# Kernel optimization log

Hardware: AMD Instinct MI355X
Metric: run time of the kernel (lower is better)

The kernel has to match this reference:

```python
import jax, jax.numpy as jnp
import numpy as np

BT, NQ, NC, C, H, HID = 192, 64, 1024, 384, 8, 1536
DH = C // H                       # 48
SCALE = DH ** -0.5
MAX_NEG = -float(np.finfo(np.float32).max)


def _ln(x, eps, g=None, b=None):
    m = x.mean(-1, keepdims=True)
    v = ((x - m) ** 2).mean(-1, keepdims=True)
    y = (x - m) / jnp.sqrt(v + eps)
    if g is not None:
        y = y * g + b
    return y


def _gelu_tanh(x):
    # GELU(approximate='tanh')
    return 0.5 * x * (1.0 + jnp.tanh(jnp.sqrt(2.0 / jnp.pi) * (x + 0.044715 * x ** 3)))


def setup_inputs() -> dict:
    key = jax.random.key(0)
    ks = jax.random.split(key, 10)
    s = lambda fan: 1.0 / np.sqrt(fan)
    return {
        "x": jax.random.normal(ks[0], (BT, NQ, C), jnp.float32),
        "context": jax.random.normal(ks[1], (BT, NC, C), jnp.float32),
        "mask": jax.random.randint(ks[2], (BT, NQ), 0, 2) > 0,
        "Wq": jax.random.normal(ks[3], (C, C), jnp.float32) * s(C),
        "bq": jnp.zeros((C,), jnp.float32),
        "Wkv": jax.random.normal(ks[4], (C, 2 * C), jnp.float32) * s(C),
        "bkv": jnp.zeros((2 * C,), jnp.float32),
        "Wo": jax.random.normal(ks[5], (C, C), jnp.float32) * s(C),
        "bo": jnp.zeros((C,), jnp.float32),
        "g_ctx": jnp.ones((C,), jnp.float32),
        "b_ctx": jnp.zeros((C,), jnp.float32),
        "W1": jax.random.normal(ks[6], (C, HID), jnp.float32) * s(C),
        "b1": jnp.zeros((HID,), jnp.float32),
        "W2": jax.random.normal(ks[7], (HID, C), jnp.float32) * s(HID),
        "b2": jnp.zeros((C,), jnp.float32),
    }


def reference(x, context, mask, Wq, bq, Wkv, bkv, Wo, bo, g_ctx, b_ctx, W1, b1, W2, b2):
    # --- cross-attention branch ---
    xn = _ln(x, 1e-6)                       # norm1 (no affine)
    cn = _ln(context, 1e-5, g_ctx, b_ctx)   # norm_context (affine, default eps)
    q = (xn @ Wq + bq).reshape(BT, NQ, H, DH).transpose(0, 2, 1, 3)    # (B,H,NQ,DH)
    kv = cn @ Wkv + bkv
    k, v = jnp.split(kv, 2, axis=-1)
    k = k.reshape(BT, NC, H, DH).transpose(0, 2, 1, 3)                 # (B,H,NC,DH)
    v = v.reshape(BT, NC, H, DH).transpose(0, 2, 1, 3)
    sim = jnp.einsum('bhqd,bhkd->bhqk', q, k) * SCALE                  # (B,H,NQ,NC)
    # mask shape (BT, NQ): True = keep query row; ~mask * (-max) bias
    bias = jnp.where(mask[:, None, :, None], 0.0, MAX_NEG)
    attn = jax.nn.softmax(sim + bias, axis=-1)
    o = jnp.einsum('bhqk,bhkd->bhqd', attn, v).transpose(0, 2, 1, 3).reshape(BT, NQ, C)
    x = x + o @ Wo + bo
    # --- MLP branch ---
    xn2 = _ln(x, 1e-6)                      # norm2 (no affine)
    x = x + _gelu_tanh(xn2 @ W1 + b1) @ W2 + b2
    return x
```

## Files before the change

kernel.cpp:

```cpp
#include <hip/hip_runtime.h>
#include <hip/hip_bf16.h>
#include <math.h>

typedef unsigned int  u32;
typedef unsigned short u16;
typedef unsigned char u8;

#define BTn   192
#define NQn   64
#define NCn   1024
#define Cd    384
#define Hn    8
#define DHn   48
#define HIDn  1536
#define ROWSX (BTn*NQn)
#define ROWSC (BTn*NCn)
#define ATT_SCALE 0.14433756729740643f

typedef __bf16 bf16x8 __attribute__((ext_vector_type(8)));
typedef float  f32x4  __attribute__((ext_vector_type(4)));

#define GLL16(gp, lp) __builtin_amdgcn_global_load_lds( \
    (const __attribute__((address_space(1))) void*)(gp), \
    (__attribute__((address_space(3))) void*)(lp), 16, 0, 0)

__device__ __forceinline__ float bf2f(u32 u) {
  union { u32 i; float f; } v; v.i = u << 16; return v.f;
}
__device__ __forceinline__ u16 f2bf(float f) {
  union { float f; u32 i; } v; v.f = f;
  u32 x = v.i;
  x += 0x7fffu + ((x >> 16) & 1u);
  return (u16)(x >> 16);
}
__device__ __forceinline__ void decode8(uint4 r, float* v) {
  v[0]=bf2f(r.x & 0xffffu); v[1]=bf2f(r.x >> 16);
  v[2]=bf2f(r.y & 0xffffu); v[3]=bf2f(r.y >> 16);
  v[4]=bf2f(r.z & 0xffffu); v[5]=bf2f(r.z >> 16);
  v[6]=bf2f(r.w & 0xffffu); v[7]=bf2f(r.w >> 16);
}
__device__ __forceinline__ float gelu_f(float x) {
  float x3 = x*x*x;
  float z = 0.7978845608028654f*x + 0.035677408136300125f*x3;
  float e = __expf(2.f*z);
  float th = 1.f - 2.f/(e+1.f);
  return 0.5f*x*(1.f+th);
}

__global__ void decode_mask_kernel(const u8* __restrict__ m, u8* __restrict__ keep) {
  __shared__ int flags[3];
  int t = threadIdx.x;
  if (t < 3) flags[t] = 0;
  __syncthreads();
  int nonbin = 0, oddset = 0, low01 = 0;
  for (int i = t; i < ROWSX; i += 256) {
    u32 b = m[i];
    if (b > 1u) nonbin = 1;
    if ((i & 3) && b) oddset = 1;
    if (((i & 3) < 2) && b) low01 = 1;
  }
  if (nonbin) flags[0] = 1;
  if (oddset) flags[1] = 1;
  if (low01)  flags[2] = 1;
  __syncthreads();
  int mode = flags[0] ? (flags[2] ? 2 : 3) : (flags[1] ? 1 : 0);
  for (int i = t; i < ROWSX; i += 256) {
    u8 k;
    if (mode == 2)      k = (m[2*i] | m[2*i+1]) ? 1 : 0;
    else if (mode == 3) k = (((const float*)m)[i] != 0.f) ? 1 : 0;
    else if (mode == 1) k = m[i] ? 1 : 0;
    else                k = (((const int*)m)[i] != 0) ? 1 : 0;
    keep[i] = k;
  }
}

template<int AFF, int SRCF32>
__global__ __launch_bounds__(256) void lnorm_kernel(
    const void* __restrict__ srcv, const float* __restrict__ gw,
    const float* __restrict__ bw, u16* __restrict__ dst, float eps)
{
  const int row  = blockIdx.x * 4 + (threadIdx.x >> 6);
  const int lane = threadIdx.x & 63;
  float v[6];
  if (SRCF32) {
    const float2* p = (const float2*)((const float*)srcv + (size_t)row*Cd);
    #pragma unroll
    for (int i = 0; i < 3; i++) { float2 u = p[lane + 64*i]; v[2*i]=u.x; v[2*i+1]=u.y; }
  } else {
    const u32* p = (const u32*)((const u16*)srcv + (size_t)row*Cd);
    #pragma unroll
    for (int i = 0; i < 3; i++) { u32 u = p[lane + 64*i]; v[2*i]=bf2f(u&0xffffu); v[2*i+1]=bf2f(u>>16); }
  }
  float s  = v[0]+v[1]+v[2]+v[3]+v[4]+v[5];
  float s2 = v[0]*v[0]+v[1]*v[1]+v[2]*v[2]+v[3]*v[3]+v[4]*v[4]+v[5]*v[5];
  #pragma unroll
  for (int o = 32; o >= 1; o >>= 1) { s += __shfl_xor(s, o); s2 += __shfl_xor(s2, o); }
  float mean = s * (1.0f/Cd);
  float var  = s2 * (1.0f/Cd) - mean*mean;
  var = var > 0.f ? var : 0.f;
  float rstd = rsqrtf(var + eps);
  u32* d32 = (u32*)(dst + (size_t)row*Cd);
  #pragma unroll
  for (int i = 0; i < 3; i++) {
    float y0 = (v[2*i]   - mean) * rstd;
    float y1 = (v[2*i+1] - mean) * rstd;
    if (AFF) {
      float2 gg = *(const float2*)(gw + 2*(lane + 64*i));
      float2 bb = *(const float2*)(bw + 2*(lane + 64*i));
      y0 = y0*gg.x + bb.x;
      y1 = y1*gg.y + bb.y;
    }
    d32[lane + 64*i] = (u32)f2bf(y0) | ((u32)f2bf(y1) << 16);
  }
}

struct WPack {
  const float* W[5];
  u16* WT[5];
  int K[5];
  int N[5];
  int off[6];
};
__global__ __launch_bounds__(256) void wconvt_all_kernel(WPack p) {
  __shared__ u16 tile[64][66];
  const int bid = blockIdx.x;
  int s = 0;
  #pragma unroll
  for (int i = 1; i < 5; i++) if (bid >= p.off[i]) s = i;
  const float* W = p.W[s];
  u16* WT = p.WT[s];
  const int K = p.K[s], N = p.N[s];
  const int lb = bid - p.off[s];
  const int t  = threadIdx.x;
  const int nt = N >> 6;
  const int bk = lb / nt, bn = lb % nt;
  const int q  = t >> 6;
  const int nl = t & 63;
  #pragma unroll
  for (int r = 0; r < 16; r++) {
    int k = q*16 + r;
    tile[nl][k] = f2bf(W[(size_t)(bk*64 + k)*N + bn*64 + nl]);
  }
  __syncthreads();
  #pragma unroll
  for (int r = 0; r < 16; r++) {
    int n = q*16 + r;
    WT[(size_t)(bn*64 + n)*K + bk*64 + nl] = tile[n][nl];
  }
}

template<int GEL, int RES, int RF32, int OF32>
__global__ __launch_bounds__(256) void mgemm_kernel(
    const u16* __restrict__ A, const u16* __restrict__ WT,
    const float* __restrict__ bias, const void* __restrict__ resv,
    void* __restrict__ Coutv, int M, int N, int K, int nx)
{
  __shared__ u16 As[3][4096];
  __shared__ u16 Bs[3][4096];
  const int t = threadIdx.x;
  const int w = t >> 6, l = t & 63, l15 = l & 15, g = l >> 4;

  const int nwg = gridDim.x;
  const int bid = blockIdx.x;
  const int wg  = (bid & 7) * (nwg >> 3) + (bid >> 3);
  const int n0 = (wg % nx) * 128, m0 = (wg / nx) * 128;
  const int wm = (w & 1) * 64, wn = (w >> 1) * 64;

  const int arow = t >> 2;
  const int swk  = (t >> 3) & 3;
  const int acol = ((t & 3) ^ swk) * 8;
  const u16* Ag = A  + (size_t)(m0 + arow) * K + acol;
  const u16* Wg = WT + (size_t)(n0 + arow) * K + acol;
  const size_t rowskip = (size_t)64 * K;

  const int xk   = (l15 >> 1) & 3;
  const int goff = ((g ^ xk) << 3);

  f32x4 acc[4][4];
  #pragma unroll
  for (int i = 0; i < 4; i++)
    #pragma unroll
    for (int j = 0; j < 4; j++) acc[i][j] = (f32x4){0.f, 0.f, 0.f, 0.f};

  const int nIter = K >> 5;

#define STAGE(nb, kk) do { \
    GLL16(Ag + (kk),           &As[nb][t*8]); \
    GLL16(Ag + (kk) + rowskip, &As[nb][2048 + t*8]); \
    GLL16(Wg + (kk),           &Bs[nb][t*8]); \
    GLL16(Wg + (kk) + rowskip, &Bs[nb][2048 + t*8]); \
  } while (0)

#define BODY(BUF, IT) do { \
    const int it_ = (IT); \
    if (it_ + 2 < nIter) { \
      STAGE((BUF + 2) % 3, (it_ + 2) << 5); \
      asm volatile("s_waitcnt vmcnt(8)" ::: "memory"); \
    } else if (it_ + 1 < nIter) { \
      asm volatile("s_waitcnt vmcnt(4)" ::: "memory"); \
    } else { \
      asm volatile("s_waitcnt vmcnt(0)" ::: "memory"); \
    } \
    __builtin_amdgcn_s_barrier(); \
    __builtin_amdgcn_sched_barrier(0); \
    { \
      bf16x8 af[4], bfv[4]; \
      _Pragma("unroll") \
      for (int i = 0; i < 4; i++) \
        af[i] = *(const bf16x8*)&As[BUF][(wm + i*16 + l15)*32 + goff]; \
      _Pragma("unroll") \
      for (int j = 0; j < 4; j++) \
        bfv[j] = *(const bf16x8*)&Bs[BUF][(wn + j*16 + l15)*32 + goff]; \
      _Pragma("unroll") \
      for (int i = 0; i < 4; i++) \
        _Pragma("unroll") \
        for (int j = 0; j < 4; j++) \
          acc[i][j] = __builtin_amdgcn_mfma_f32_16x16x32_bf16(bfv[j], af[i], acc[i][j], 0, 0, 0); \
    } \
    __builtin_amdgcn_sched_barrier(0); \
    __builtin_amdgcn_s_barrier(); \
  } while (0)

  STAGE(0, 0);
  STAGE(1, 32);
  for (int it0 = 0; it0 < nIter; it0 += 3) {
    BODY(0, it0);
    BODY(1, it0 + 1);
    BODY(2, it0 + 2);
  }
#undef BODY
#undef STAGE

  const float* resf = (const float*)resv;
  const u16*   resb = (const u16*)resv;
  float* Cf = (float*)Coutv;
  u16*   Cb = (u16*)Coutv;
  #pragma unroll
  for (int j = 0; j < 4; j++) {
    const int nb = n0 + wn + j*16 + g*4;
    const float4 bv = *(const float4*)&bias[nb];
    #pragma unroll
    for (int i = 0; i < 4; i++) {
      const int m = m0 + wm + i*16 + l15;
      float c0 = acc[i][j][0] + bv.x;
      float c1 = acc[i][j][1] + bv.y;
      float c2 = acc[i][j][2] + bv.z;
      float c3 = acc[i][j][3] + bv.w;
      if (GEL) { c0 = gelu_f(c0); c1 = gelu_f(c1); c2 = gelu_f(c2); c3 = gelu_f(c3); }
      if (RES) {
        if (RF32) {
          float4 r = *(const float4*)&resf[(size_t)m*N + nb];
          c0 += r.x; c1 += r.y; c2 += r.z; c3 += r.w;
        } else {
          uint2 r = *(const uint2*)&resb[(size_t)m*N + nb];
          c0 += bf2f(r.x & 0xffffu); c1 += bf2f(r.x >> 16);
          c2 += bf2f(r.y & 0xffffu); c3 += bf2f(r.y >> 16);
        }
      }
      if (OF32) {
        *(float4*)&Cf[(size_t)m*N + nb] = make_float4(c0, c1, c2, c3);
      } else {
        uint2 pk = make_uint2((u32)f2bf(c0) | ((u32)f2bf(c1) << 16),
                              (u32)f2bf(c2) | ((u32)f2bf(c3) << 16));
        *(uint2*)&Cb[(size_t)m*N + nb] = pk;
      }
    }
  }
}

template<int GEL, int RES, int RF32, int OF32>
__global__ __launch_bounds__(512, 4) void mgemm256_kernel(
    const u16* __restrict__ A, const u16* __restrict__ WT,
    const float* __restrict__ bias, const void* __restrict__ resv,
    void* __restrict__ Coutv, int M, int N, int K, int nx)
{
  __shared__ u16 As[3][4096];
  __shared__ u16 Bs[3][8192];
  const int t = threadIdx.x;
  const int w = t >> 6, l = t & 63, l15 = l & 15, g = l >> 4;

  const int nwg = gridDim.x;
  const int bid = blockIdx.x;
  const int wg  = (bid & 7) * (nwg >> 3) + (bid >> 3);
  const int n0 = (wg % nx) * 256, m0 = (wg / nx) * 128;
  const int wm = (w & 1) * 64, wn = (w >> 1) * 64;

  const int arow = t >> 2;
  const int swk  = (t >> 3) & 3;
  const int acol = ((t & 3) ^ swk) * 8;
  const u16* Ag = A  + (size_t)(m0 + arow) * K + acol;
  const u16* Wg = WT + (size_t)(n0 + arow) * K + acol;
  const size_t rowskipB = (size_t)128 * K;

  const int xk   = (l15 >> 1) & 3;
  const int goff = ((g ^ xk) << 3);

  f32x4 acc[4][4];
  #pragma unroll
  for (int i = 0; i < 4; i++)
    #pragma unroll
    for (int j = 0; j < 4; j++) acc[i][j] = (f32x4){0.f, 0.f, 0.f, 0.f};

  const int nIter = K >> 5;

#define STAGE(nb, kk) do { \
    GLL16(Ag + (kk),            &As[nb][t*8]); \
    GLL16(Wg + (kk),            &Bs[nb][t*8]); \
    GLL16(Wg + (kk) + rowskipB, &Bs[nb][4096 + t*8]); \
  } while (0)

#define BODY(BUF, IT) do { \
    const int it_ = (IT); \
    if (it_ + 2 < nIter) { \
      STAGE((BUF + 2) % 3, (it_ + 2) << 5); \
      asm volatile("s_waitcnt vmcnt(6)" ::: "memory"); \
    } else if (it_ + 1 < nIter) { \
      asm volatile("s_waitcnt vmcnt(3)" ::: "memory"); \
    } else { \
      asm volatile("s_waitcnt vmcnt(0)" ::: "memory"); \
    } \
    __builtin_amdgcn_s_barrier(); \
    __builtin_amdgcn_sched_barrier(0); \
    { \
      bf16x8 af[4], bfv[4]; \
      _Pragma("unroll") \
      for (int i = 0; i < 4; i++) \
        af[i] = *(const bf16x8*)&As[BUF][(wm + i*16 + l15)*32 + goff]; \
      _Pragma("unroll") \
      for (int j = 0; j < 4; j++) \
        bfv[j] = *(const bf16x8*)&Bs[BUF][(wn + j*16 + l15)*32 + goff]; \
      _Pragma("unroll") \
      for (int i = 0; i < 4; i++) \
        _Pragma("unroll") \
        for (int j = 0; j < 4; j++) \
          acc[i][j] = __builtin_amdgcn_mfma_f32_16x16x32_bf16(bfv[j], af[i], acc[i][j], 0, 0, 0); \
    } \
    __builtin_amdgcn_sched_barrier(0); \
    __builtin_amdgcn_s_barrier(); \
  } while (0)

  STAGE(0, 0);
  STAGE(1, 32);
  for (int it0 = 0; it0 < nIter; it0 += 3) {
    BODY(0, it0);
    BODY(1, it0 + 1);
    BODY(2, it0 + 2);
  }
#undef BODY
#undef STAGE

  const float* resf = (const float*)resv;
  const u16*   resb = (const u16*)resv;
  float* Cf = (float*)Coutv;
  u16*   Cb = (u16*)Coutv;
  #pragma unroll
  for (int j = 0; j < 4; j++) {
    const int nb = n0 + wn + j*16 + g*4;
    const float4 bv = *(const float4*)&bias[nb];
    #pragma unroll
    for (int i = 0; i < 4; i++) {
      const int m = m0 + wm + i*16 + l15;
      float c0 = acc[i][j][0] + bv.x;
      float c1 = acc[i][j][1] + bv.y;
      float c2 = acc[i][j][2] + bv.z;
      float c3 = acc[i][j][3] + bv.w;
      if (GEL) { c0 = gelu_f(c0); c1 = gelu_f(c1); c2 = gelu_f(c2); c3 = gelu_f(c3); }
      if (RES) {
        if (RF32) {
          float4 r = *(const float4*)&resf[(size_t)m*N + nb];
          c0 += r.x; c1 += r.y; c2 += r.z; c3 += r.w;
        } else {
          uint2 r = *(const uint2*)&resb[(size_t)m*N + nb];
          c0 += bf2f(r.x & 0xffffu); c1 += bf2f(r.x >> 16);
          c2 += bf2f(r.y & 0xffffu); c3 += bf2f(r.y >> 16);
        }
      }
      if (OF32) {
        *(float4*)&Cf[(size_t)m*N + nb] = make_float4(c0, c1, c2, c3);
      } else {
        uint2 pk = make_uint2((u32)f2bf(c0) | ((u32)f2bf(c1) << 16),
                              (u32)f2bf(c2) | ((u32)f2bf(c3) << 16));
        *(uint2*)&Cb[(size_t)m*N + nb] = pk;
      }
    }
  }
}

__global__ __launch_bounds__(256) void fattn_kernel(
    const u16* __restrict__ qb, const u16* __restrict__ kvb,
    const u8* __restrict__ keep, u16* __restrict__ ob)
{
  __shared__ u16 Qs[64*72];
  __shared__ u16 Ks[64*72];
  __shared__ u16 Vt[48*72];
  __shared__ u16 Ps[4][16*72];

  const int t = threadIdx.x;
  const int w = t >> 6, l = t & 63, l15 = l & 15, g = l >> 4;
  const int h = blockIdx.x, b = blockIdx.y;
  const int wq = w * 16;
  const int krow0 = t / 6, kp0 = t % 6;
  const int krow1 = (256 + t) / 6, kp1 = (256 + t) % 6;
  const int vdq = (t >> 4) * 4, vkq = (t & 15) * 4;

  for (int i = t; i < 2304; i += 256) { ((u32*)Qs)[i] = 0; ((u32*)Ks)[i] = 0; }
  __syncthreads();

  for (int i = t; i < 384; i += 256) {
    int row = i / 6, p = i % 6;
    uint4 v4 = *(const uint4*)(qb + (size_t)(b*NQn + row)*Cd + h*DHn + p*8);
    float f[8]; decode8(v4, f);
    u16 e[8];
    #pragma unroll
    for (int j = 0; j < 8; j++) e[j] = f2bf(f[j] * ATT_SCALE);
    uint4 pk = make_uint4((u32)e[0] | ((u32)e[1] << 16), (u32)e[2] | ((u32)e[3] << 16),
                          (u32)e[4] | ((u32)e[5] << 16), (u32)e[6] | ((u32)e[7] << 16));
    *(uint4*)&Qs[row*72 + p*8] = pk;
  }

  u32 kw = *(const u32*)&keep[b*NQn + wq + g*4];
  float kf[4];
  #pragma unroll
  for (int r = 0; r < 4; r++) kf[r] = ((kw >> (8*r)) & 0xffu) ? 1.f : 0.f;

  float mrow[4], lrow[4];
  f32x4 oacc[3];
  #pragma unroll
  for (int r = 0; r < 4; r++) { mrow[r] = kf[r] > 0.f ? -3.0e38f : 0.f; lrow[r] = 0.f; }
  #pragma unroll
  for (int d = 0; d < 3; d++) oacc[d] = (f32x4){0.f, 0.f, 0.f, 0.f};

  auto loadKV = [&](int kt, uint4& KR0, uint4& KR1, uint2* V) {
    const u16* base = kvb + ((size_t)b*NCn + (size_t)kt*64) * (2*(size_t)Cd);
    KR0 = *(const uint4*)(base + (size_t)krow0*(2*Cd) + h*DHn + kp0*8);
    if (t < 128)
      KR1 = *(const uint4*)(base + (size_t)krow1*(2*Cd) + h*DHn + kp1*8);
    if (t < 192) {
      const u16* vs = base + (size_t)vkq*(2*Cd) + Cd + h*DHn + vdq;
      V[0] = *(const uint2*)(vs);
      V[1] = *(const uint2*)(vs + 2*Cd);
      V[2] = *(const uint2*)(vs + 4*Cd);
      V[3] = *(const uint2*)(vs + 6*Cd);
    }
  };
  auto writeKV = [&](const uint4& KR0, const uint4& KR1, const uint2* V) {
    *(uint4*)&Ks[krow0*72 + kp0*8] = KR0;
    if (t < 128) *(uint4*)&Ks[krow1*72 + kp1*8] = KR1;
    if (t < 192) {
      #pragma unroll
      for (int jj = 0; jj < 4; jj++) {
        u16 o4[4] = {((const u16*)&V[0])[jj], ((const u16*)&V[1])[jj],
                     ((const u16*)&V[2])[jj], ((const u16*)&V[3])[jj]};
        *(uint2*)&Vt[(vdq+jj)*72 + vkq] = *(uint2*)o4;
      }
    }
  };

  bf16x8 qf0, qf1;
  auto compute = [&]() {
    f32x4 sf[4];
    #pragma unroll
    for (int f = 0; f < 4; f++) {
      bf16x8 ka = *(const bf16x8*)&Ks[(f*16 + l15)*72 + g*8];
      bf16x8 kb = *(const bf16x8*)&Ks[(f*16 + l15)*72 + 32 + g*8];
      f32x4 z = (f32x4){0.f, 0.f, 0.f, 0.f};
      z = __builtin_amdgcn_mfma_f32_16x16x32_bf16(qf0, ka, z, 0, 0, 0);
      sf[f] = __builtin_amdgcn_mfma_f32_16x16x32_bf16(qf1, kb, z, 0, 0, 0);
    }
    float p[4][4], pmax[4];
    #pragma unroll
    for (int r = 0; r < 4; r++) {
      float pm = fmaxf(fmaxf(sf[0][r], sf[1][r]), fmaxf(sf[2][r], sf[3][r]));
      #pragma unroll
      for (int s = 1; s < 16; s <<= 1) pm = fmaxf(pm, __shfl_xor(pm, s));
      pmax[r] = pm;
    }
    float dm = fmaxf(fmaxf(kf[0]*(pmax[0]-mrow[0]), kf[1]*(pmax[1]-mrow[1])),
                     fmaxf(kf[2]*(pmax[2]-mrow[2]), kf[3]*(pmax[3]-mrow[3])));
    if (!__all(dm <= 8.f)) {
      #pragma unroll
      for (int r = 0; r < 4; r++) {
        float mn = kf[r] > 0.f ? fmaxf(mrow[r], pmax[r]) : 0.f;
        float sc = kf[r] > 0.f ? __expf(mrow[r] - mn) : 1.f;
        mrow[r] = mn;
        lrow[r] *= sc;
        oacc[0][r] *= sc; oacc[1][r] *= sc; oacc[2][r] *= sc;
      }
    }
    #pragma unroll
    for (int r = 0; r < 4; r++) {
      float p0 = kf[r] > 0.f ? __expf(sf[0][r] - mrow[r]) : 1.f;
      float p1 = kf[r] > 0.f ? __expf(sf[1][r] - mrow[r]) : 1.f;
      float p2 = kf[r] > 0.f ? __expf(sf[2][r] - mrow[r]) : 1.f;
      float p3 = kf[r] > 0.f ? __expf(sf[3][r] - mrow[r]) : 1.f;
      p[0][r]=p0; p[1][r]=p1; p[2][r]=p2; p[3][r]=p3;
      float ps = p0+p1+p2+p3;
      #pragma unroll
      for (int s = 1; s < 16; s <<= 1) ps += __shfl_xor(ps, s);
      lrow[r] += ps;
    }
    #pragma unroll
    for (int f = 0; f < 4; f++)
      #pragma unroll
      for (int r = 0; r < 4; r++)
        Ps[w][(g*4 + r)*72 + f*16 + l15] = f2bf(p[f][r]);
    bf16x8 pa0 = *(const bf16x8*)&Ps[w][l15*72 + g*8];
    bf16x8 pa1 = *(const bf16x8*)&Ps[w][l15*72 + 32 + g*8];
    #pragma unroll
    for (int df = 0; df < 3; df++) {
      bf16x8 vb0 = *(const bf16x8*)&Vt[(df*16 + l15)*72 + g*8];
      bf16x8 vb1 = *(const bf16x8*)&Vt[(df*16 + l15)*72 + 32 + g*8];
      oacc[df] = __builtin_amdgcn_mfma_f32_16x16x32_bf16(pa0, vb0, oacc[df], 0, 0, 0);
      oacc[df] = __builtin_amdgcn_mfma_f32_16x16x32_bf16(pa1, vb1, oacc[df], 0, 0, 0);
    }
  };

  uint4 ka0, ka1, kb0_, kb1_;
  uint2 va[4], vb_[4];
  loadKV(0, ka0, ka1, va);
  __syncthreads();

  qf0 = *(const bf16x8*)&Qs[(wq + l15)*72 + g*8];
  qf1 = *(const bf16x8*)&Qs[(wq + l15)*72 + 32 + g*8];

  for (int kt = 0; kt < 16; kt += 2) {
    writeKV(ka0, ka1, va);
    asm volatile("s_waitcnt lgkmcnt(0)" ::: "memory");
    __builtin_amdgcn_sched_barrier(0);
    __builtin_amdgcn_s_barrier();
    __builtin_amdgcn_sched_barrier(0);
    loadKV(kt + 1, kb0_, kb1_, vb_);
    compute();
    __builtin_amdgcn_sched_barrier(0);
    __builtin_amdgcn_s_barrier();
    writeKV(kb0_, kb1_, vb_);
    asm volatile("s_waitcnt lgkmcnt(0)" ::: "memory");
    __builtin_amdgcn_sched_barrier(0);
    __builtin_amdgcn_s_barrier();
    __builtin_amdgcn_sched_barrier(0);
    if (kt + 2 < 16) loadKV(kt + 2, ka0, ka1, va);
    compute();
    if (kt + 2 < 16) {
      __builtin_amdgcn_sched_barrier(0);
      __builtin_amdgcn_s_barrier();
    }
  }

  #pragma unroll
  for (int r = 0; r < 4; r++) {
    float inv = 1.f / lrow[r];
    size_t qrow = (size_t)(b*NQn + wq + g*4 + r);
    #pragma unroll
    for (int df = 0; df < 3; df++)
      ob[qrow*Cd + h*DHn + df*16 + l15] = f2bf(oacc[df][r] * inv);
  }
}

extern "C" void kernel_launch(void* const* d_in, const int* in_sizes, int n_in,
                              void* d_out, int out_size, void* d_ws, size_t ws_size,
                              hipStream_t stream) {
  (void)in_sizes; (void)n_in; (void)out_size; (void)ws_size;
  const float* x   = (const float*)d_in[0];
  const float* ctx = (const float*)d_in[1];
  const u8*    msk = (const u8*)   d_in[2];
  const float* Wq  = (const float*)d_in[3];
  const float* bq  = (const float*)d_in[4];
  const float* Wkv = (const float*)d_in[5];
  const float* bkv = (const float*)d_in[6];
  const float* Wo  = (const float*)d_in[7];
  const float* bo  = (const float*)d_in[8];
  const float* gc  = (const float*)d_in[9];
  const float* bc  = (const float*)d_in[10];
  const float* W1  = (const float*)d_in[11];
  const float* b1  = (const float*)d_in[12];
  const float* W2  = (const float*)d_in[13];
  const float* b2  = (const float*)d_in[14];
  float* out = (float*)d_out;

  char* ws = (char*)d_ws;
  size_t off = 0;
  auto bump = [&](size_t bytes) -> size_t {
    size_t o = off; off += (bytes + 255) & ~(size_t)255; return o;
  };
  const size_t act = (size_t)ROWSX * Cd * 2;
  size_t o_keep = bump(ROWSX);
  size_t o_xn   = bump(act);
  size_t o_x1n  = bump(act);
  size_t o_q    = bump(act);
  size_t o_ob   = bump(act);
  size_t o_x1   = bump(act);
  size_t o_hid  = bump((size_t)ROWSX * HIDn * 2);
  size_t o_wtq  = bump((size_t)Cd*Cd*2);
  size_t o_wtkv = bump((size_t)Cd*2*Cd*2);
  size_t o_wto  = bump((size_t)Cd*Cd*2);
  size_t o_wt1  = bump((size_t)Cd*HIDn*2);
  size_t o_wt2  = bump((size_t)HIDn*Cd*2);
  size_t o_cn   = bump((size_t)ROWSC * Cd * 2);
  size_t o_kv   = bump((size_t)ROWSC * 2 * Cd * 2);

  u8*  keep = (u8*)(ws + o_keep);
  u16* xn   = (u16*)(ws + o_xn);
  u16* x1n  = (u16*)(ws + o_x1n);
  u16* qb   = (u16*)(ws + o_q);
  u16* obuf = (u16*)(ws + o_ob);
  u16* x1b  = (u16*)(ws + o_x1);
  u16* hidb = (u16*)(ws + o_hid);
  u16* wtq  = (u16*)(ws + o_wtq);
  u16* wtkv = (u16*)(ws + o_wtkv);
  u16* wto  = (u16*)(ws + o_wto);
  u16* wt1  = (u16*)(ws + o_wt1);
  u16* wt2  = (u16*)(ws + o_wt2);
  u16* cnb  = (u16*)(ws + o_cn);
  u16* kvb  = (u16*)(ws + o_kv);

  decode_mask_kernel<<<1, 256, 0, stream>>>(msk, keep);

  WPack wp;
  wp.W[0]=Wq;  wp.WT[0]=wtq;  wp.K[0]=Cd;   wp.N[0]=Cd;
  wp.W[1]=Wkv; wp.WT[1]=wtkv; wp.K[1]=Cd;   wp.N[1]=2*Cd;
  wp.W[2]=Wo;  wp.WT[2]=wto;  wp.K[2]=Cd;   wp.N[2]=Cd;
  wp.W[3]=W1;  wp.WT[3]=wt1;  wp.K[3]=Cd;   wp.N[3]=HIDn;
  wp.W[4]=W2;  wp.WT[4]=wt2;  wp.K[4]=HIDn; wp.N[4]=Cd;
  wp.off[0]=0; wp.off[1]=36; wp.off[2]=108; wp.off[3]=144; wp.off[4]=288; wp.off[5]=432;
  wconvt_all_kernel<<<432, 256, 0, stream>>>(wp);

  lnorm_kernel<0,1><<<ROWSX/4, 256, 0, stream>>>(x, nullptr, nullptr, xn, 1e-6f);

  mgemm_kernel<0,0,0,0><<<3*(ROWSX/128), 256, 0, stream>>>(
      xn, wtq, bq, nullptr, qb, ROWSX, Cd, Cd, 3);

  lnorm_kernel<1,1><<<ROWSC/4, 256, 0, stream>>>(ctx, gc, bc, cnb, 1e-5f);
  mgemm256_kernel<0,0,0,0><<<3*(ROWSC/128), 512, 0, stream>>>(
      cnb, wtkv, bkv, nullptr, kvb, ROWSC, 2*Cd, Cd, 3);
  fattn_kernel<<<dim3(Hn, BTn), 256, 0, stream>>>(qb, kvb, keep, obuf);

  mgemm_kernel<0,1,1,0><<<3*(ROWSX/128), 256, 0, stream>>>(
      obuf, wto, bo, x, x1b, ROWSX, Cd, Cd, 3);

  lnorm_kernel<0,0><<<ROWSX/4, 256, 0, stream>>>(x1b, nullptr, nullptr, x1n, 1e-6f);

  mgemm256_kernel<1,0,0,0><<<6*(ROWSX/128), 512, 0, stream>>>(
      x1n, wt1, b1, nullptr, hidb, ROWSX, HIDn, Cd, 6);

  mgemm_kernel<0,1,0,1><<<3*(ROWSX/128), 256, 0, stream>>>(
      hidb, wt2, b2, x1b, out, ROWSX, Cd, HIDn, 3);
}
```

Baseline: 589.1 us.

## Chunk context LN/KV/attention by batch, double-buffer GEMMs, fold scale into Q GEMM

The context layernorm, KV projection and attention now run in two batch chunks of 96, so the cn/kv intermediates are half the size and more likely to stay resident in the last-level cache between producer and consumer. Both GEMM kernels drop from triple to double buffering in LDS, which frees shared memory per block but leaves less latency hiding. The attention scale is applied in the Q-projection epilogue instead of being re-quantised when the attention kernel loads Q. In exchange there are extra kernel launches and smaller grids per chunk.

```diff
diff --git a/kernel.cpp b/kernel.cpp
--- a/kernel.cpp
+++ b/kernel.cpp
@@ -16,6 +16,7 @@
 #define ROWSX (BTn*NQn)
 #define ROWSC (BTn*NCn)
 #define ATT_SCALE 0.14433756729740643f
+#define CBc   96
 
 typedef __bf16 bf16x8 __attribute__((ext_vector_type(8)));
 typedef float  f32x4  __attribute__((ext_vector_type(4)));
@@ -149,14 +150,14 @@
   }
 }
 
-template<int GEL, int RES, int RF32, int OF32>
+template<int GEL, int RES, int RF32, int OF32, int SCL>
 __global__ __launch_bounds__(256) void mgemm_kernel(
     const u16* __restrict__ A, const u16* __restrict__ WT,
     const float* __restrict__ bias, const void* __restrict__ resv,
     void* __restrict__ Coutv, int M, int N, int K, int nx)
 {
-  __shared__ u16 As[3][4096];
-  __shared__ u16 Bs[3][4096];
+  __shared__ u16 As[2][4096];
+  __shared__ u16 Bs[2][4096];
   const int t = threadIdx.x;
   const int w = t >> 6, l = t & 63, l15 = l & 15, g = l >> 4;
 
@@ -193,10 +194,8 @@
 
 #define BODY(BUF, IT) do { \
     const int it_ = (IT); \
-    if (it_ + 2 < nIter) { \
-      STAGE((BUF + 2) % 3, (it_ + 2) << 5); \
-      asm volatile("s_waitcnt vmcnt(8)" ::: "memory"); \
-    } else if (it_ + 1 < nIter) { \
+    if (it_ + 1 < nIter) { \
+      STAGE(BUF ^ 1, (it_ + 1) << 5); \
       asm volatile("s_waitcnt vmcnt(4)" ::: "memory"); \
     } else { \
       asm volatile("s_waitcnt vmcnt(0)" ::: "memory"); \
@@ -222,11 +221,124 @@
   } while (0)
 
   STAGE(0, 0);
-  STAGE(1, 32);
-  for (int it0 = 0; it0 < nIter; it0 += 3) {
-    BODY(0, it0);
-    BODY(1, it0 + 1);
-    BODY(2, it0 + 2);
+  for (int it = 0; it < nIter; it += 2) {
+    BODY(0, it);
+    BODY(1, it + 1);
+  }
+#undef BODY
+#undef STAGE
+
+  const float* resf = (const float*)resv;
+  const u16*   resb = (const u16*)resv;
+  float* Cf = (float*)Coutv;
+  u16*   Cb = (u16*)Coutv;
+  #pragma unroll
+  for (int j = 0; j < 4; j++) {
+    const int nb = n0 + wn + j*16 + g*4;
+    const float4 bv = *(const float4*)&bias[nb];
+    #pragma unroll
+    for (int i = 0; i < 4; i++) {
+      const int m = m0 + wm + i*16 + l15;
+      float c0 = acc[i][j][0] + bv.x;
+      float c1 = acc[i][j][1] + bv.y;
+      float c2 = acc[i][j][2] + bv.z;
+      float c3 = acc[i][j][3] + bv.w;
+      if (SCL) { c0 *= ATT_SCALE; c1 *= ATT_SCALE; c2 *= ATT_SCALE; c3 *= ATT_SCALE; }
+      if (GEL) { c0 = gelu_f(c0); c1 = gelu_f(c1); c2 = gelu_f(c2); c3 = gelu_f(c3); }
+      if (RES) {
+        if (RF32) {
+          float4 r = *(const float4*)&resf[(size_t)m*N + nb];
+          c0 += r.x; c1 += r.y; c2 += r.z; c3 += r.w;
+        } else {
+          uint2 r = *(const uint2*)&resb[(size_t)m*N + nb];
+          c0 += bf2f(r.x & 0xffffu); c1 += bf2f(r.x >> 16);
+          c2 += bf2f(r.y & 0xffffu); c3 += bf2f(r.y >> 16);
+        }
+      }
+      if (OF32) {
+        *(float4*)&Cf[(size_t)m*N + nb] = make_float4(c0, c1, c2, c3);
+      } else {
+        uint2 pk = make_uint2((u32)f2bf(c0) | ((u32)f2bf(c1) << 16),
+                              (u32)f2bf(c2) | ((u32)f2bf(c3) << 16));
+        *(uint2*)&Cb[(size_t)m*N + nb] = pk;
+      }
+    }
+  }
+}
+
+template<int GEL, int RES, int RF32, int OF32>
+__global__ __launch_bounds__(512, 4) void mgemm256_kernel(
+    const u16* __restrict__ A, const u16* __restrict__ WT,
+    const float* __restrict__ bias, const void* __restrict__ resv,
+    void* __restrict__ Coutv, int M, int N, int K, int nx)
+{
+  __shared__ u16 As[2][4096];
+  __shared__ u16 Bs[2][8192];
+  const int t = threadIdx.x;
+  const int w = t >> 6, l = t & 63, l15 = l & 15, g = l >> 4;
+
+  const int nwg = gridDim.x;
+  const int bid = blockIdx.x;
+  const int wg  = (bid & 7) * (nwg >> 3) + (bid >> 3);
+  const int n0 = (wg % nx) * 256, m0 = (wg / nx) * 128;
+  const int wm = (w & 1) * 64, wn = (w >> 1) * 64;
+
+  const int arow = t >> 2;
+  const int swk  = (t >> 3) & 3;
+  const int acol = ((t & 3) ^ swk) * 8;
+  const u16* Ag = A  + (size_t)(m0 + arow) * K + acol;
+  const u16* Wg = WT + (size_t)(n0 + arow) * K + acol;
+  const size_t rowskipB = (size_t)128 * K;
+
+  const int xk   = (l15 >> 1) & 3;
+  const int goff = ((g ^ xk) << 3);
+
+  f32x4 acc[4][4];
+  #pragma unroll
+  for (int i = 0; i < 4; i++)
+    #pragma unroll
+    for (int j = 0; j < 4; j++) acc[i][j] = (f32x4){0.f, 0.f, 0.f, 0.f};
+
+  const int nIter = K >> 5;
+
+#define STAGE(nb, kk) do { \
+    GLL16(Ag + (kk),            &As[nb][t*8]); \
+    GLL16(Wg + (kk),            &Bs[nb][t*8]); \
+    GLL16(Wg + (kk) + rowskipB, &Bs[nb][4096 + t*8]); \
+  } while (0)
+
+#define BODY(BUF, IT) do { \
+    const int it_ = (IT); \
+    if (it_ + 1 < nIter) { \
+      STAGE(BUF ^ 1, (it_ + 1) << 5); \
+      asm volatile("s_waitcnt vmcnt(3)" ::: "memory"); \
+    } else { \
+      asm volatile("s_waitcnt vmcnt(0)" ::: "memory"); \
+    } \
+    __builtin_amdgcn_s_barrier(); \
+    __builtin_amdgcn_sched_barrier(0); \
+    { \
+      bf16x8 af[4], bfv[4]; \
+      _Pragma("unroll") \
+      for (int i = 0; i < 4; i++) \
+        af[i] = *(const bf16x8*)&As[BUF][(wm + i*16 + l15)*32 + goff]; \
+      _Pragma("unroll") \
+      for (int j = 0; j < 4; j++) \
+        bfv[j] = *(const bf16x8*)&Bs[BUF][(wn + j*16 + l15)*32 + goff]; \
+      _Pragma("unroll") \
+      for (int i = 0; i < 4; i++) \
+        _Pragma("unroll") \
+        for (int j = 0; j < 4; j++) \
+          acc[i][j] = __builtin_amdgcn_mfma_f32_16x16x32_bf16(bfv[j], af[i], acc[i][j], 0, 0, 0); \
+    } \
+    __builtin_amdgcn_sched_barrier(0); \
+    __builtin_amdgcn_s_barrier(); \
+  } while (0)
+
+  STAGE(0, 0);
+  for (int it = 0; it < nIter; it += 2) {
+    BODY(0, it);
+    BODY(1, it + 1);
   }
 #undef BODY
 #undef STAGE
@@ -268,127 +380,9 @@
   }
 }
 
-template<int GEL, int RES, int RF32, int OF32>
-__global__ __launch_bounds__(512, 4) void mgemm256_kernel(
-    const u16* __restrict__ A, const u16* __restrict__ WT,
-    const float* __restrict__ bias, const void* __restrict__ resv,
-    void* __restrict__ Coutv, int M, int N, int K, int nx)
-{
-  __shared__ u16 As[3][4096];
-  __shared__ u16 Bs[3][8192];
-  const int t = threadIdx.x;
-  const int w = t >> 6, l = t & 63, l15 = l & 15, g = l >> 4;
-
-  const int nwg = gridDim.x;
-  const int bid = blockIdx.x;
-  const int wg  = (bid & 7) * (nwg >> 3) + (bid >> 3);
-  const int n0 = (wg % nx) * 256, m0 = (wg / nx) * 128;
-  const int wm = (w & 1) * 64, wn = (w >> 1) * 64;
-
-  const int arow = t >> 2;
-  const int swk  = (t >> 3) & 3;
-  const int acol = ((t & 3) ^ swk) * 8;
-  const u16* Ag = A  + (size_t)(m0 + arow) * K + acol;
-  const u16* Wg = WT + (size_t)(n0 + arow) * K + acol;
-  const size_t rowskipB = (size_t)128 * K;
-
-  const int xk   = (l15 >> 1) & 3;
-  const int goff = ((g ^ xk) << 3);
-
-  f32x4 acc[4][4];
-  #pragma unroll
-  for (int i = 0; i < 4; i++)
-    #pragma unroll
-    for (int j = 0; j < 4; j++) acc[i][j] = (f32x4){0.f, 0.f, 0.f, 0.f};
-
-  const int nIter = K >> 5;
-
-#define STAGE(nb, kk) do { \
-    GLL16(Ag + (kk),            &As[nb][t*8]); \
-    GLL16(Wg + (kk),            &Bs[nb][t*8]); \
-    GLL16(Wg + (kk) + rowskipB, &Bs[nb][4096 + t*8]); \
-  } while (0)
-
-#define BODY(BUF, IT) do { \
-    const int it_ = (IT); \
-    if (it_ + 2 < nIter) { \
-      STAGE((BUF + 2) % 3, (it_ + 2) << 5); \
-      asm volatile("s_waitcnt vmcnt(6)" ::: "memory"); \
-    } else if (it_ + 1 < nIter) { \
-      asm volatile("s_waitcnt vmcnt(3)" ::: "memory"); \
-    } else { \
-      asm volatile("s_waitcnt vmcnt(0)" ::: "memory"); \
-    } \
-    __builtin_amdgcn_s_barrier(); \
-    __builtin_amdgcn_sched_barrier(0); \
-    { \
-      bf16x8 af[4], bfv[4]; \
-      _Pragma("unroll") \
-      for (int i = 0; i < 4; i++) \
-        af[i] = *(const bf16x8*)&As[BUF][(wm + i*16 + l15)*32 + goff]; \
-      _Pragma("unroll") \
-      for (int j = 0; j < 4; j++) \
-        bfv[j] = *(const bf16x8*)&Bs[BUF][(wn + j*16 + l15)*32 + goff]; \
-      _Pragma("unroll") \
-      for (int i = 0; i < 4; i++) \
-        _Pragma("unroll") \
-        for (int j = 0; j < 4; j++) \
-          acc[i][j] = __builtin_amdgcn_mfma_f32_16x16x32_bf16(bfv[j], af[i], acc[i][j], 0, 0, 0); \
-    } \
-    __builtin_amdgcn_sched_barrier(0); \
-    __builtin_amdgcn_s_barrier(); \
-  } while (0)
-
-  STAGE(0, 0);
-  STAGE(1, 32);
-  for (int it0 = 0; it0 < nIter; it0 += 3) {
-    BODY(0, it0);
-    BODY(1, it0 + 1);
-    BODY(2, it0 + 2);
-  }
-#undef BODY
-#undef STAGE
-
-  const float* resf = (const float*)resv;
-  const u16*   resb = (const u16*)resv;
-  float* Cf = (float*)Coutv;
-  u16*   Cb = (u16*)Coutv;
-  #pragma unroll
-  for (int j = 0; j < 4; j++) {
-    const int nb = n0 + wn + j*16 + g*4;
-    const float4 bv = *(const float4*)&bias[nb];
-    #pragma unroll
-    for (int i = 0; i < 4; i++) {
-      const int m = m0 + wm + i*16 + l15;
-      float c0 = acc[i][j][0] + bv.x;
-      float c1 = acc[i][j][1] + bv.y;
-      float c2 = acc[i][j][2] + bv.z;
-      float c3 = acc[i][j][3] + bv.w;
-      if (GEL) { c0 = gelu_f(c0); c1 = gelu_f(c1); c2 = gelu_f(c2); c3 = gelu_f(c3); }
-      if (RES) {
-        if (RF32) {
-          float4 r = *(const float4*)&resf[(size_t)m*N + nb];
-          c0 += r.x; c1 += r.y; c2 += r.z; c3 += r.w;
-        } else {
-          uint2 r = *(const uint2*)&resb[(size_t)m*N + nb];
-          c0 += bf2f(r.x & 0xffffu); c1 += bf2f(r.x >> 16);
-          c2 += bf2f(r.y & 0xffffu); c3 += bf2f(r.y >> 16);
-        }
-      }
-      if (OF32) {
-        *(float4*)&Cf[(size_t)m*N + nb] = make_float4(c0, c1, c2, c3);
-      } else {
-        uint2 pk = make_uint2((u32)f2bf(c0) | ((u32)f2bf(c1) << 16),
-                              (u32)f2bf(c2) | ((u32)f2bf(c3) << 16));
-        *(uint2*)&Cb[(size_t)m*N + nb] = pk;
-      }
-    }
-  }
-}
-
 __global__ __launch_bounds__(256) void fattn_kernel(
     const u16* __restrict__ qb, const u16* __restrict__ kvb,
-    const u8* __restrict__ keep, u16* __restrict__ ob)
+    const u8* __restrict__ keep, u16* __restrict__ ob, int b0)
 {
   __shared__ u16 Qs[64*72];
   __shared__ u16 Ks[64*72];
@@ -397,7 +391,8 @@
 
   const int t = threadIdx.x;
   const int w = t >> 6, l = t & 63, l15 = l & 15, g = l >> 4;
-  const int h = blockIdx.x, b = blockIdx.y;
+  const int h = blockIdx.x, bz = blockIdx.y;
+  const int b = b0 + bz;
   const int wq = w * 16;
   const int krow0 = t / 6, kp0 = t % 6;
   const int krow1 = (256 + t) / 6, kp1 = (256 + t) % 6;
@@ -408,14 +403,8 @@
 
   for (int i = t; i < 384; i += 256) {
     int row = i / 6, p = i % 6;
-    uint4 v4 = *(const uint4*)(qb + (size_t)(b*NQn + row)*Cd + h*DHn + p*8);
-    float f[8]; decode8(v4, f);
-    u16 e[8];
-    #pragma unroll
-    for (int j = 0; j < 8; j++) e[j] = f2bf(f[j] * ATT_SCALE);
-    uint4 pk = make_uint4((u32)e[0] | ((u32)e[1] << 16), (u32)e[2] | ((u32)e[3] << 16),
-                          (u32)e[4] | ((u32)e[5] << 16), (u32)e[6] | ((u32)e[7] << 16));
-    *(uint4*)&Qs[row*72 + p*8] = pk;
+    *(uint4*)&Qs[row*72 + p*8] =
+        *(const uint4*)(qb + (size_t)(b*NQn + row)*Cd + h*DHn + p*8);
   }
 
   u32 kw = *(const u32*)&keep[b*NQn + wq + g*4];
@@ -431,7 +420,7 @@
   for (int d = 0; d < 3; d++) oacc[d] = (f32x4){0.f, 0.f, 0.f, 0.f};
 
   auto loadKV = [&](int kt, uint4& KR0, uint4& KR1, uint2* V) {
-    const u16* base = kvb + ((size_t)b*NCn + (size_t)kt*64) * (2*(size_t)Cd);
+    const u16* base = kvb + ((size_t)bz*NCn + (size_t)kt*64) * (2*(size_t)Cd);
     KR0 = *(const uint4*)(base + (size_t)krow0*(2*Cd) + h*DHn + kp0*8);
     if (t < 128)
       KR1 = *(const uint4*)(base + (size_t)krow1*(2*Cd) + h*DHn + kp1*8);
@@ -595,8 +584,8 @@
   size_t o_wto  = bump((size_t)Cd*Cd*2);
   size_t o_wt1  = bump((size_t)Cd*HIDn*2);
   size_t o_wt2  = bump((size_t)HIDn*Cd*2);
-  size_t o_cn   = bump((size_t)ROWSC * Cd * 2);
-  size_t o_kv   = bump((size_t)ROWSC * 2 * Cd * 2);
+  size_t o_cn   = bump((size_t)CBc * NCn * Cd * 2);
+  size_t o_kv   = bump((size_t)CBc * NCn * 2 * Cd * 2);
 
   u8*  keep = (u8*)(ws + o_keep);
   u16* xn   = (u16*)(ws + o_xn);
@@ -626,15 +615,18 @@
 
   lnorm_kernel<0,1><<<ROWSX/4, 256, 0, stream>>>(x, nullptr, nullptr, xn, 1e-6f);
 
-  mgemm_kernel<0,0,0,0><<<3*(ROWSX/128), 256, 0, stream>>>(
+  mgemm_kernel<0,0,0,0,1><<<3*(ROWSX/128), 256, 0, stream>>>(
       xn, wtq, bq, nullptr, qb, ROWSX, Cd, Cd, 3);
 
-  lnorm_kernel<1,1><<<ROWSC/4, 256, 0, stream>>>(ctx, gc, bc, cnb, 1e-5f);
-  mgemm256_kernel<0,0,0,0><<<3*(ROWSC/128), 512, 0, stream>>>(
-      cnb, wtkv, bkv, nullptr, kvb, ROWSC, 2*Cd, Cd, 3);
-  fattn_kernel<<<dim3(Hn, BTn), 256, 0, stream>>>(qb, kvb, keep, obuf);
-
-  mgemm_kernel<0,1,1,0><<<3*(ROWSX/128), 256, 0, stream>>>(
+  for (int b0 = 0; b0 < BTn; b0 += CBc) {
+    lnorm_kernel<1,1><<<CBc*NCn/4, 256, 0, stream>>>(
+        ctx + (size_t)b0*NCn*Cd, gc, bc, cnb, 1e-5f);
+    mgemm256_kernel<0,0,0,0><<<3*(CBc*NCn/128), 512, 0, stream>>>(
+        cnb, wtkv, bkv, nullptr, kvb, CBc*NCn, 2*Cd, Cd, 3);
+    fattn_kernel<<<dim3(Hn, CBc), 256, 0, stream>>>(qb, kvb, keep, obuf, b0);
+  }
+
+  mgemm_kernel<0,1,1,0,0><<<3*(ROWSX/128), 256, 0, stream>>>(
       obuf, wto, bo, x, x1b, ROWSX, Cd, Cd, 3);
 
   lnorm_kernel<0,0><<<ROWSX/4, 256, 0, stream>>>(x1b, nullptr, nullptr, x1n, 1e-6f);
@@ -642,6 +634,6 @@
   mgemm256_kernel<1,0,0,0><<<6*(ROWSX/128), 512, 0, stream>>>(
       x1n, wt1, b1, nullptr, hidb, ROWSX, HIDn, Cd, 6);
 
-  mgemm_kernel<0,1,0,1><<<3*(ROWSX/128), 256, 0, stream>>>(
+  mgemm_kernel<0,1,0,1,0><<<3*(ROWSX/128), 256, 0, stream>>>(
       hidb, wt2, b2, x1b, out, ROWSX, Cd, HIDn, 3);
 }
```

Result: no change. 585.2 us (-0.7%).
